# Performance work log

Measured on AMD Instinct MI355X. Metric: run time of the kernel, lower is better.

Reference implementation:

```python
import jax, jax.numpy as jnp
import numpy as np

MIN_LEVEL, MAX_LEVEL = 3, 7
IMG = 1024
BASE_SIZE = 4
RATIOS = (0.5, 1.0, 2.0)
LO, HI = 0.4, 0.5  # min_iou_thresh, max_iou_thresh


def _make_anchors():
    outs, sizes = [], []
    for lvl in range(MIN_LEVEL, MAX_LEVEL + 1):
        stride = 2 ** lvl
        size = BASE_SIZE * stride
        anch = []
        for r in RATIOS:
            h = size * np.sqrt(r)
            w = size / np.sqrt(r)
            anch.append([-w / 2, -h / 2, w / 2, h / 2])
        anch = np.array(anch, np.float32)                      # [A,4]
        n = IMG // stride
        c = (np.arange(n, dtype=np.float32) + 0.5) * stride
        sx, sy = np.meshgrid(c, c)
        shifts = np.stack([sx, sy, sx, sy], -1).reshape(-1, 1, 4)
        lvl_anch = (shifts + anch[None]).reshape(-1, 4)        # [n*n*A,4]
        outs.append(lvl_anch)
        sizes.append(lvl_anch.shape[0])
    return np.concatenate(outs, 0).astype(np.float32), sizes

ANCHORS_NP, LEVEL_SIZES = _make_anchors()   # total 65472 anchors, sizes [49152,12288,3072,768,192]


def _pair_iou(anch, g):
    # anch [N,4], g [G,4] -> IoU [N,G]
    x1 = jnp.maximum(anch[:, None, 0], g[None, :, 0])
    y1 = jnp.maximum(anch[:, None, 1], g[None, :, 1])
    x2 = jnp.minimum(anch[:, None, 2], g[None, :, 2])
    y2 = jnp.minimum(anch[:, None, 3], g[None, :, 3])
    inter = jnp.clip(x2 - x1, 0.0) * jnp.clip(y2 - y1, 0.0)
    aa = (anch[:, 2] - anch[:, 0]) * (anch[:, 3] - anch[:, 1])
    ag = (g[:, 2] - g[:, 0]) * (g[:, 3] - g[:, 1])
    return inter / (aa[:, None] + ag[None, :] - inter + 1e-9)


def _bbox_transform(anch, gt):
    # anchor/gt boxes [...,4] (x1,y1,x2,y2) -> (dx,dy,dw,dh)
    aw = anch[..., 2] - anch[..., 0]
    ah = anch[..., 3] - anch[..., 1]
    ax = anch[..., 0] + 0.5 * aw
    ay = anch[..., 1] + 0.5 * ah
    gw = gt[..., 2] - gt[..., 0]
    gh = gt[..., 3] - gt[..., 1]
    gx = gt[..., 0] + 0.5 * gw
    gy = gt[..., 1] + 0.5 * gh
    return jnp.stack([(gx - ax) / aw, (gy - ay) / ah,
                      jnp.log(gw / aw), jnp.log(gh / ah)], -1)


def setup_inputs() -> dict:
    key = jax.random.key(0)
    k1, k2, k3, k4 = jax.random.split(key, 4)
    B, G = 16, 32
    cx = jax.random.uniform(k1, (B, G), minval=64.0, maxval=960.0)
    cy = jax.random.uniform(k2, (B, G), minval=64.0, maxval=960.0)
    hw = jax.random.uniform(k3, (B, G), minval=8.0, maxval=150.0)
    hh = jax.random.uniform(k4, (B, G), minval=8.0, maxval=150.0)
    bb_coord = jnp.stack([jnp.clip(cx - hw, 0, IMG), jnp.clip(cy - hh, 0, IMG),
                          jnp.clip(cx + hw, 0, IMG), jnp.clip(cy + hh, 0, IMG)], -1).astype(jnp.float32)
    bird_ids = jax.random.randint(jax.random.fold_in(key, 1), (B, G), 1, 81, dtype=jnp.int32)
    anchors = jnp.asarray(ANCHORS_NP)
    return {"bb_coord": bb_coord, "bird_ids": bird_ids, "anchors": anchors}


def reference(bb_coord, bird_ids, anchors):
    # bb_coord [B,G,4] float, bird_ids [B,G] int, anchors [N_total,4] float
    B, G = bird_ids.shape
    offs = np.cumsum([0] + LEVEL_SIZES)
    # IoUs per level: [B,N_l,G]
    per = []
    for li in range(len(LEVEL_SIZES)):
        anch = anchors[offs[li]:offs[li + 1]]
        ov = jax.vmap(lambda g: _pair_iou(anch, g))(bb_coord)
        per.append((anch, ov))
    # best level per GT (argmax of per-level best anchor IoU)
    gt_max = jnp.stack([ov.max(axis=1) for _, ov in per], 0)     # [L,B,G]
    gt_max_level = jnp.argmax(gt_max, axis=0)                    # [B,G]
    bidx = jnp.arange(B)[:, None]
    labels_all, regs_all = [], []
    for li, (anch, ov) in enumerate(per):
        N = anch.shape[0]
        max_ov = ov.max(axis=2)                                  # [B,N]
        arg = jnp.argmax(ov, axis=2)                             # [B,N]
        assigned_box = bb_coord[bidx, arg]                       # [B,N,4]
        assigned_id = bird_ids[bidx, arg]                        # [B,N]
        gt_arg = jnp.argmax(ov, axis=1)                          # [B,G] best anchor per GT
        sel = gt_max_level == li                                 # GTs forced onto this level
        sidx = jnp.where(sel, gt_arg, N)                         # scatter to pad slot N when unselected
        ab = jnp.concatenate([assigned_box, jnp.zeros((B, 1, 4), bb_coord.dtype)], 1)
        ab = ab.at[bidx, sidx].set(bb_coord)[:, :N]
        ai = jnp.concatenate([assigned_id, jnp.zeros((B, 1), bird_ids.dtype)], 1)
        ai = ai.at[bidx, sidx].set(bird_ids)[:, :N]
        pos = jnp.concatenate([max_ov >= HI, jnp.zeros((B, 1), bool)], 1)
        pos = pos.at[bidx, sidx].set(True)[:, :N]
        ign = (max_ov >= LO) & (max_ov < HI)
        label = jnp.where(pos, ai, jnp.where(ign, -1, 0)).astype(jnp.int32)
        reg = jnp.where(pos[..., None], _bbox_transform(anch[None], ab), 0.0)
        labels_all.append(label)
        regs_all.append(reg)
    return jnp.concatenate(labels_all, 1), jnp.concatenate(regs_all, 1)
```

## Files before the change

### kernel.cpp

```cpp
#include <hip/hip_runtime.h>

#pragma clang fp contract(off)

#define A_TOTAL 65472
#define NB 16
#define NG 32
#define NLVL 5


__global__ __launch_bounds__(256) void fused_kernel(
    const float* __restrict__ bb,
    const int* __restrict__ ids,
    const float* __restrict__ anchors,
    unsigned long long* __restrict__ part,
    float* __restrict__ out)
{
    const int wid = threadIdx.x >> 6;
    const int lane = threadIdx.x & 63;
    const int b = blockIdx.x >> 6;
    const int r = ((blockIdx.x & 63) << 2) + wid;
    const int start = r << 8;
    const bool full = (r != 255);
    const int lvl = (r < 192) ? 0 : (r < 240) ? 1 : (r < 252) ? 2 : (r < 255) ? 3 : 4;

    __shared__ float4 sbb[NG];
    __shared__ float sag[NG];
    __shared__ int sid[NG];
    if (threadIdx.x < NG) {
        float4 q = ((const float4*)bb)[b * NG + threadIdx.x];
        sbb[threadIdx.x] = q;
        sag[threadIdx.x] = (q.z - q.x) * (q.w - q.y);
        sid[threadIdx.x] = ids[b * NG + threadIdx.x];
    }
    __syncthreads();

    float abest[4];
    int   agid[4];
#pragma unroll
    for (int k = 0; k < 4; ++k) { abest[k] = -1.0f; agid[k] = 0; }

    unsigned long long red = 0ull;

#pragma unroll
    for (int h = 0; h < 2; ++h) {
        unsigned long long key[16];
#pragma unroll
        for (int gi = 0; gi < 16; ++gi) key[gi] = 0ull;

#pragma unroll
        for (int k = 0; k < 4; ++k) {
            if (k == 3 && !full) continue;
            const int n = start + (k << 6) + lane;
            const float4 an = ((const float4*)anchors)[n];
            const float aa = (an.z - an.x) * (an.w - an.y);
#pragma unroll
            for (int gi = 0; gi < 16; ++gi) {
                const int g = h * 16 + gi;
                const float4 q = sbb[g];
                float x1 = fmaxf(an.x, q.x);
                float y1 = fmaxf(an.y, q.y);
                float x2 = fminf(an.z, q.z);
                float y2 = fminf(an.w, q.w);
                float w  = fmaxf(x2 - x1, 0.0f);
                float hh = fmaxf(y2 - y1, 0.0f);
                float inter = w * hh;
                float denom = aa + sag[g] - inter + 1e-9f;
                float v = inter / denom;
                unsigned long long kk =
                    ((unsigned long long)__float_as_uint(v) << 32) |
                    (unsigned long long)(~(unsigned int)n);
                if (kk > key[gi]) key[gi] = kk;
                if (v > abest[k]) { abest[k] = v; agid[k] = g; }
            }
        }
#pragma unroll
        for (int gi = 0; gi < 16; ++gi) {
            unsigned long long kx = key[gi];
#pragma unroll
            for (int s = 1; s < 64; s <<= 1) {
                unsigned long long o = __shfl_xor(kx, s, 64);
                kx = (o > kx) ? o : kx;
            }
            if (lane == h * 16 + gi) red = kx;
        }
    }
    if (lane < NG) {
        atomicMax(&part[(b * NG + lane) * NLVL + lvl], red);
    }

#pragma unroll
    for (int k = 0; k < 4; ++k) {
        if (k == 3 && !full) continue;
        const int n = start + (k << 6) + lane;
        const float4 an = ((const float4*)anchors)[n];
        float label;
        float4 rg;
        if (abest[k] >= 0.5f) {
            const float4 gtb = sbb[agid[k]];
            label = (float)sid[agid[k]];
            float aw = an.z - an.x;
            float ah = an.w - an.y;
            float ax = an.x + 0.5f * aw;
            float ay = an.y + 0.5f * ah;
            float gw = gtb.z - gtb.x;
            float gh = gtb.w - gtb.y;
            float gx = gtb.x + 0.5f * gw;
            float gy = gtb.y + 0.5f * gh;
            rg = make_float4((gx - ax) / aw, (gy - ay) / ah, logf(gw / aw), logf(gh / ah));
        } else {
            label = (abest[k] >= 0.4f) ? -1.0f : 0.0f;
            rg = make_float4(0.0f, 0.0f, 0.0f, 0.0f);
        }
        out[b * A_TOTAL + n] = label;
        ((float4*)(out + NB * A_TOTAL))[b * A_TOTAL + n] = rg;
    }
}

__global__ void reduce_kernel(const unsigned long long* __restrict__ part,
                              int* __restrict__ forced)
{
    const int i = threadIdx.x;
    if (i >= NB * NG) return;
    const unsigned long long* p = part + i * NLVL;
    unsigned long long k0 = p[0];
    unsigned int bestf = (unsigned int)(k0 >> 32);
    unsigned long long bestk = k0;
#pragma unroll
    for (int l = 1; l < NLVL; ++l) {
        unsigned long long kl = p[l];
        unsigned int f = (unsigned int)(kl >> 32);
        if (f > bestf) { bestf = f; bestk = kl; }
    }
    forced[i] = (int)(~(unsigned int)(bestk & 0xFFFFFFFFull));
}

__global__ void fixup_kernel(const float* __restrict__ bb,
                             const int* __restrict__ ids,
                             const float* __restrict__ anchors,
                             const int* __restrict__ forced,
                             float* __restrict__ out)
{
    const int b = threadIdx.x;
    if (b >= NB) return;
    for (int g = 0; g < NG; ++g) {
        const int n = forced[b * NG + g];
        const float4 gtb = ((const float4*)bb)[b * NG + g];
        const float4 an = ((const float4*)anchors)[n];
        float aw = an.z - an.x;
        float ah = an.w - an.y;
        float ax = an.x + 0.5f * aw;
        float ay = an.y + 0.5f * ah;
        float gw = gtb.z - gtb.x;
        float gh = gtb.w - gtb.y;
        float gx = gtb.x + 0.5f * gw;
        float gy = gtb.y + 0.5f * gh;
        out[b * A_TOTAL + n] = (float)ids[b * NG + g];
        ((float4*)(out + NB * A_TOTAL))[b * A_TOTAL + n] =
            make_float4((gx - ax) / aw, (gy - ay) / ah, logf(gw / aw), logf(gh / ah));
    }
}

extern "C" void kernel_launch(void* const* d_in, const int* in_sizes, int n_in,
                              void* d_out, int out_size, void* d_ws, size_t ws_size,
                              hipStream_t stream) {
    const float* bb      = (const float*)d_in[0];
    const int*   ids     = (const int*)d_in[1];
    const float* anchors = (const float*)d_in[2];
    float* out = (float*)d_out;

    unsigned long long* part = (unsigned long long*)d_ws;
    int* forced = (int*)((char*)d_ws + NB * NG * NLVL * sizeof(unsigned long long));

    hipMemsetAsync(part, 0, NB * NG * NLVL * sizeof(unsigned long long), stream);
    hipLaunchKernelGGL(fused_kernel, dim3(NB * 64), dim3(256), 0, stream,
                       bb, ids, anchors, part, out);
    hipLaunchKernelGGL(reduce_kernel, dim3(1), dim3(512), 0, stream, part, forced);
    hipLaunchKernelGGL(fixup_kernel, dim3(1), dim3(64), 0, stream,
                       bb, ids, anchors, forced, out);
}
```

Before: 133.2 us.

## Halve per-wave anchors, loop GTs with scalar keys, merge reduce and fixup kernels

Each wave now covers 128 anchors instead of 256 and the grid doubles, which is meant to raise parallelism and occupancy. The GT loop is rolled, keeping one 64-bit key per GT instead of a 16-entry key array, which lowers register pressure at the cost of a shuffle reduction per GT. Anchors are loaded once and reused for the label pass. The reduce and fixup kernels are merged into one 512-thread kernel that parallelises fixup per (batch, GT) and resolves duplicate forced anchors by letting the last GT win, which removes a launch and the serial per-batch loop.

```diff
diff --git a/kernel.cpp b/kernel.cpp
--- a/kernel.cpp
+++ b/kernel.cpp
@@ -15,17 +15,17 @@
     unsigned long long* __restrict__ part,
     float* __restrict__ out)
 {
-    const int wid = threadIdx.x >> 6;
+    const int wid  = threadIdx.x >> 6;
     const int lane = threadIdx.x & 63;
-    const int b = blockIdx.x >> 6;
-    const int r = ((blockIdx.x & 63) << 2) + wid;
-    const int start = r << 8;
-    const bool full = (r != 255);
-    const int lvl = (r < 192) ? 0 : (r < 240) ? 1 : (r < 252) ? 2 : (r < 255) ? 3 : 4;
+    const int b = blockIdx.x >> 7;
+    const int w = ((blockIdx.x & 127) << 2) + wid;
+    const int start = w << 7;
+    const bool full = (w != 511);
+    const int lvl = (w < 384) ? 0 : (w < 480) ? 1 : (w < 504) ? 2 : (w < 510) ? 3 : 4;
 
     __shared__ float4 sbb[NG];
-    __shared__ float sag[NG];
-    __shared__ int sid[NG];
+    __shared__ float  sag[NG];
+    __shared__ int    sid[NG];
     if (threadIdx.x < NG) {
         float4 q = ((const float4*)bb)[b * NG + threadIdx.x];
         sbb[threadIdx.x] = q;
@@ -34,74 +34,68 @@
     }
     __syncthreads();
 
-    float abest[4];
-    int   agid[4];
-#pragma unroll
-    for (int k = 0; k < 4; ++k) { abest[k] = -1.0f; agid[k] = 0; }
+    float4 an[2];
+    float  aa[2];
+    an[0] = ((const float4*)anchors)[start + lane];
+    aa[0] = (an[0].z - an[0].x) * (an[0].w - an[0].y);
+    if (full) {
+        an[1] = ((const float4*)anchors)[start + 64 + lane];
+        aa[1] = (an[1].z - an[1].x) * (an[1].w - an[1].y);
+    } else {
+        an[1] = an[0]; aa[1] = aa[0];
+    }
 
+    float abest[2] = {-1.0f, -1.0f};
+    int   agid[2]  = {0, 0};
     unsigned long long red = 0ull;
 
+    for (int g = 0; g < NG; ++g) {
+        const float4 q  = sbb[g];
+        const float  ag = sag[g];
+        unsigned long long key = 0ull;
 #pragma unroll
-    for (int h = 0; h < 2; ++h) {
-        unsigned long long key[16];
-#pragma unroll
-        for (int gi = 0; gi < 16; ++gi) key[gi] = 0ull;
-
-#pragma unroll
-        for (int k = 0; k < 4; ++k) {
-            if (k == 3 && !full) continue;
-            const int n = start + (k << 6) + lane;
-            const float4 an = ((const float4*)anchors)[n];
-            const float aa = (an.z - an.x) * (an.w - an.y);
-#pragma unroll
-            for (int gi = 0; gi < 16; ++gi) {
-                const int g = h * 16 + gi;
-                const float4 q = sbb[g];
-                float x1 = fmaxf(an.x, q.x);
-                float y1 = fmaxf(an.y, q.y);
-                float x2 = fminf(an.z, q.z);
-                float y2 = fminf(an.w, q.w);
-                float w  = fmaxf(x2 - x1, 0.0f);
-                float hh = fmaxf(y2 - y1, 0.0f);
-                float inter = w * hh;
-                float denom = aa + sag[g] - inter + 1e-9f;
-                float v = inter / denom;
-                unsigned long long kk =
-                    ((unsigned long long)__float_as_uint(v) << 32) |
-                    (unsigned long long)(~(unsigned int)n);
-                if (kk > key[gi]) key[gi] = kk;
-                if (v > abest[k]) { abest[k] = v; agid[k] = g; }
-            }
+        for (int k = 0; k < 2; ++k) {
+            if (k == 1 && !full) continue;
+            const unsigned int n = (unsigned int)(start + (k << 6) + lane);
+            float x1 = fmaxf(an[k].x, q.x);
+            float y1 = fmaxf(an[k].y, q.y);
+            float x2 = fminf(an[k].z, q.z);
+            float y2 = fminf(an[k].w, q.w);
+            float ww = fmaxf(x2 - x1, 0.0f);
+            float hh = fmaxf(y2 - y1, 0.0f);
+            float inter = ww * hh;
+            float denom = aa[k] + ag - inter + 1e-9f;
+            float v = inter / denom;
+            unsigned long long kk =
+                ((unsigned long long)__float_as_uint(v) << 32) |
+                (unsigned long long)(~n);
+            if (kk > key) key = kk;
+            if (v > abest[k]) { abest[k] = v; agid[k] = g; }
         }
 #pragma unroll
-        for (int gi = 0; gi < 16; ++gi) {
-            unsigned long long kx = key[gi];
-#pragma unroll
-            for (int s = 1; s < 64; s <<= 1) {
-                unsigned long long o = __shfl_xor(kx, s, 64);
-                kx = (o > kx) ? o : kx;
-            }
-            if (lane == h * 16 + gi) red = kx;
+        for (int s = 1; s < 64; s <<= 1) {
+            unsigned long long o = __shfl_xor(key, s, 64);
+            if (o > key) key = o;
         }
+        if (lane == g) red = key;
     }
     if (lane < NG) {
         atomicMax(&part[(b * NG + lane) * NLVL + lvl], red);
     }
 
 #pragma unroll
-    for (int k = 0; k < 4; ++k) {
-        if (k == 3 && !full) continue;
+    for (int k = 0; k < 2; ++k) {
+        if (k == 1 && !full) continue;
         const int n = start + (k << 6) + lane;
-        const float4 an = ((const float4*)anchors)[n];
         float label;
         float4 rg;
         if (abest[k] >= 0.5f) {
             const float4 gtb = sbb[agid[k]];
             label = (float)sid[agid[k]];
-            float aw = an.z - an.x;
-            float ah = an.w - an.y;
-            float ax = an.x + 0.5f * aw;
-            float ay = an.y + 0.5f * ah;
+            float aw = an[k].z - an[k].x;
+            float ah = an[k].w - an[k].y;
+            float ax = an[k].x + 0.5f * aw;
+            float ay = an[k].y + 0.5f * ah;
             float gw = gtb.z - gtb.x;
             float gh = gtb.w - gtb.y;
             float gx = gtb.x + 0.5f * gw;
@@ -116,36 +110,38 @@
     }
 }
 
-__global__ void reduce_kernel(const unsigned long long* __restrict__ part,
-                              int* __restrict__ forced)
+__global__ __launch_bounds__(512) void tail_kernel(
+    const float* __restrict__ bb,
+    const int* __restrict__ ids,
+    const float* __restrict__ anchors,
+    unsigned long long* __restrict__ part,
+    float* __restrict__ out)
 {
-    const int i = threadIdx.x;
-    if (i >= NB * NG) return;
-    const unsigned long long* p = part + i * NLVL;
-    unsigned long long k0 = p[0];
+    const int t = threadIdx.x;
+    __shared__ int sfor[NB * NG];
+
+    unsigned long long k0 = atomicMax(&part[t * NLVL + 0], 0ull);
     unsigned int bestf = (unsigned int)(k0 >> 32);
     unsigned long long bestk = k0;
 #pragma unroll
     for (int l = 1; l < NLVL; ++l) {
-        unsigned long long kl = p[l];
+        unsigned long long kl = atomicMax(&part[t * NLVL + l], 0ull);
         unsigned int f = (unsigned int)(kl >> 32);
         if (f > bestf) { bestf = f; bestk = kl; }
     }
-    forced[i] = (int)(~(unsigned int)(bestk & 0xFFFFFFFFull));
-}
+    const int n = (int)(~(unsigned int)(bestk & 0xFFFFFFFFull));
+    sfor[t] = n;
+    __syncthreads();
 
-__global__ void fixup_kernel(const float* __restrict__ bb,
-                             const int* __restrict__ ids,
-                             const float* __restrict__ anchors,
-                             const int* __restrict__ forced,
-                             float* __restrict__ out)
-{
-    const int b = threadIdx.x;
-    if (b >= NB) return;
-    for (int g = 0; g < NG; ++g) {
-        const int n = forced[b * NG + g];
-        const float4 gtb = ((const float4*)bb)[b * NG + g];
-        const float4 an = ((const float4*)anchors)[n];
+    const int b = t >> 5;
+    const int g = t & 31;
+    bool shadowed = false;
+    for (int g2 = g + 1; g2 < NG; ++g2)
+        if (sfor[(b << 5) | g2] == n) shadowed = true;
+
+    if (!shadowed) {
+        const float4 gtb = ((const float4*)bb)[t];
+        const float4 an  = ((const float4*)anchors)[n];
         float aw = an.z - an.x;
         float ah = an.w - an.y;
         float ax = an.x + 0.5f * aw;
@@ -154,7 +150,7 @@
         float gh = gtb.w - gtb.y;
         float gx = gtb.x + 0.5f * gw;
         float gy = gtb.y + 0.5f * gh;
-        out[b * A_TOTAL + n] = (float)ids[b * NG + g];
+        out[b * A_TOTAL + n] = (float)ids[t];
         ((float4*)(out + NB * A_TOTAL))[b * A_TOTAL + n] =
             make_float4((gx - ax) / aw, (gy - ay) / ah, logf(gw / aw), logf(gh / ah));
     }
@@ -169,12 +165,10 @@
     float* out = (float*)d_out;
 
     unsigned long long* part = (unsigned long long*)d_ws;
-    int* forced = (int*)((char*)d_ws + NB * NG * NLVL * sizeof(unsigned long long));
 
     hipMemsetAsync(part, 0, NB * NG * NLVL * sizeof(unsigned long long), stream);
-    hipLaunchKernelGGL(fused_kernel, dim3(NB * 64), dim3(256), 0, stream,
+    hipLaunchKernelGGL(fused_kernel, dim3(NB * 128), dim3(256), 0, stream,
                        bb, ids, anchors, part, out);
-    hipLaunchKernelGGL(reduce_kernel, dim3(1), dim3(512), 0, stream, part, forced);
-    hipLaunchKernelGGL(fixup_kernel, dim3(1), dim3(64), 0, stream,
-                       bb, ids, anchors, forced, out);
+    hipLaunchKernelGGL(tail_kernel, dim3(1), dim3(512), 0, stream,
+                       bb, ids, anchors, part, out);
 }
```

Measured after the change: 118.5 us. -11.0%, faster.
